# Performance work log

Measured on AMD Instinct MI355X. Metric: run time of the kernel, lower is better.

The kernel has to match this reference:

```python
import jax, jax.numpy as jnp
import numpy as np

K = 64          # number of tags, incl. BOS/EOS
V = 50000       # vocab size (excl. BOS/EOS words)
D = 128         # lexicon embedding dim
BOS_T = K - 2   # BOS tag index
EOS_T = K - 1   # EOS tag index
BATCH = 8192
L = 126         # interior words per sentence (n = L + 2 incl. BOS/EOS)
EPS = 1e-45     # smoothing added to A and B in updateAB


def setup_inputs() -> dict:
    key = jax.random.key(0)
    k1, k2, k3, k4 = jax.random.split(key, 4)
    words = jax.random.randint(k1, (BATCH, L), 0, V, dtype=jnp.int32)
    ThetaB = 0.01 * jax.random.uniform(k2, (K, D), dtype=jnp.float32)
    WA = 0.01 * jax.random.uniform(k3, (K, K), dtype=jnp.float32)
    E = jax.random.normal(k4, (V, D), dtype=jnp.float32)
    return {"words": words, "ThetaB": ThetaB, "WA": WA, "E": E}


def reference(words, ThetaB, WA, E):
    # updateAB(): A = softmax(WA) with BOS column forced to prob 0 (-inf logit)
    WAm = WA.at[:, BOS_T].set(-jnp.inf)
    A = jax.nn.softmax(WAm, axis=1) + EPS                       # [K, K]
    B = jax.nn.softmax(ThetaB @ E.T, axis=1)                    # [K, V]
    B = B.at[EOS_T, :].set(0.0).at[BOS_T, :].set(0.0) + EPS
    logA = jnp.log(A)                                           # [K, K]
    logB = jnp.log(B)                                           # [K, V]

    # Emission log-probs gathered per token: [L, B, K]
    em = jnp.swapaxes(logB.T[words], 0, 1)

    # alpha_0: one-hot (in log space) at BOS tag
    alpha0 = jnp.full((words.shape[0], K), -jnp.inf, dtype=logA.dtype)
    alpha0 = alpha0.at[:, BOS_T].set(0.0)

    def step(alpha, e):
        # alpha: [B, K] over prev tags; logsumexp over prev tag axis
        new = jax.nn.logsumexp(alpha[:, :, None] + logA[None, :, :], axis=1) + e
        return new, None

    alpha, _ = jax.lax.scan(step, alpha0, em)
    # Final transition into EOS tag (no emission): log Z per sentence, [B]
    logZ = jax.nn.logsumexp(alpha + logA[None, :, EOS_T], axis=1)
    return logZ
```

## Files before the change

kernel.cpp:

```cpp
#include <hip/hip_runtime.h>
#include <hip/hip_bf16.h>
#include <math.h>


#define KT 64
#define VV 50000
#define DD 128
#define BOS_T 62
#define EOS_T 63
#define LLEN 126
#define EPSF 1e-45f
#define SCALE_F 65536.0f
#define LOG_TOTAL_SCALE (2016.0f * 0.6931471805599453f)
#define NBLK 782
#define PBLK 784
#define TPH 21
#define NPH 6

#define BTN_OFF   0
#define A_OFF     3200000
#define SUM_OFF   3216384
#define PART_OFF  3216640

typedef short short8 __attribute__((ext_vector_type(8)));
typedef float f32x4  __attribute__((ext_vector_type(4)));
typedef float f32x2  __attribute__((ext_vector_type(2)));

union U8 { short8 v; unsigned u[4]; short s[8]; };

static __device__ inline unsigned short f2bf_u(float x) {
    __hip_bfloat16 h = __float2bfloat16(x);
    return *reinterpret_cast<unsigned short*>(&h);
}
static __device__ inline short f2bf(float x) { return (short)f2bf_u(x); }

#if __has_builtin(__builtin_amdgcn_cvt_pk_bf16_f32)
typedef __bf16 bf16x2 __attribute__((ext_vector_type(2)));
static __device__ inline unsigned pk2(float a, float b) {
    bf16x2 r = __builtin_amdgcn_cvt_pk_bf16_f32(a, b);
    return *reinterpret_cast<unsigned*>(&r);
}
#else
static __device__ inline unsigned pk2(float a, float b) {
    union { float f; unsigned u; } ua, ub;
    ua.f = a; ub.f = b;
    return ((ua.u + 0x8000u) >> 16) | ((ub.u + 0x8000u) & 0xFFFF0000u);
}
#endif
static __device__ inline float lo16(unsigned u) { union { unsigned i; float f; } c; c.i = u << 16;        return c.f; }
static __device__ inline float hi16(unsigned u) { union { unsigned i; float f; } c; c.i = u & 0xffff0000u; return c.f; }

#if __has_builtin(__builtin_amdgcn_cvt_pk_fp8_f32)
static __device__ inline unsigned pk4f8(float a, float b, float c, float d) {
    int v = __builtin_amdgcn_cvt_pk_fp8_f32(a, b, 0, false);
    v = __builtin_amdgcn_cvt_pk_fp8_f32(c, d, v, true);
    return (unsigned)v;
}
#else
static __device__ inline unsigned enc1f8(float x) {
    union { float f; unsigned u; } c; c.f = x;
    unsigned u = c.u & 0x7FFFFFFFu;
    unsigned r = u + 0x7FFFFu + ((u >> 20) & 1u);
    return ((r >> 20) - (120u << 3)) & 0x7Fu;
}
static __device__ inline unsigned pk4f8(float a, float b, float c, float d) {
    return enc1f8(a) | (enc1f8(b) << 8) | (enc1f8(c) << 16) | (enc1f8(d) << 24);
}
#endif

#if __has_builtin(__builtin_amdgcn_cvt_pk_f32_fp8)
static __device__ inline f32x2 dec2lo(unsigned w) { return __builtin_amdgcn_cvt_pk_f32_fp8((int)w, false); }
static __device__ inline f32x2 dec2hi(unsigned w) { return __builtin_amdgcn_cvt_pk_f32_fp8((int)w, true); }
#else
static __device__ inline float dec1f8(unsigned b) {
    union { unsigned u; float f; } c;
    c.u = ((b & 0x80u) << 24) | (((b & 0x7Fu) << 20) + (120u << 23));
    return c.f;
}
static __device__ inline f32x2 dec2lo(unsigned w) { f32x2 r; r.x = dec1f8(w & 0xFF); r.y = dec1f8((w >> 8) & 0xFF); return r; }
static __device__ inline f32x2 dec2hi(unsigned w) { f32x2 r; r.x = dec1f8((w >> 16) & 0xFF); r.y = dec1f8(w >> 24); return r; }
#endif

#if __has_builtin(__builtin_amdgcn_global_load_lds)
#define GLLDS(gp, lbase)                                                        \
    __builtin_amdgcn_global_load_lds(                                           \
        (__attribute__((address_space(1))) void*)const_cast<unsigned char*>(gp),\
        (__attribute__((address_space(3))) void*)(lbase), 16, 0, 0)
#else
#define GLLDS(gp, lbase)                                                        \
    do { *(uint4*)((unsigned char*)(lbase) + (threadIdx.x & 63) * 16) =         \
             *(const uint4*)(gp); } while (0)
#endif

__global__ __launch_bounds__(256) void k_emit(const float* __restrict__ ThetaB,
                                              const float* __restrict__ E,
                                              unsigned char* __restrict__ btn8,
                                              float* __restrict__ partial) {
    __shared__ float red[4][KT];
    int t    = threadIdx.x;
    int lane = t & 63;
    int w    = t >> 6;
    int n    = lane & 15;
    int q    = lane >> 4;
    int v0   = (blockIdx.x * 4 + w) * 16;

    int rowE = v0 + n;
    bool valid = rowE < VV;
    rowE = valid ? rowE : VV - 1;
    float4 ex[4][2];
#pragma unroll
    for (int kt = 0; kt < 4; ++kt) {
        const float* p = E + (size_t)rowE * DD + kt * 32 + q * 8;
        ex[kt][0] = *(const float4*)p;
        ex[kt][1] = *(const float4*)(p + 4);
    }

    short8 Th[4][4];
#pragma unroll
    for (int kt = 0; kt < 4; ++kt)
#pragma unroll
        for (int mt = 0; mt < 4; ++mt) {
            const float* p = ThetaB + (mt * 16 + n) * DD + kt * 32 + q * 8;
            float4 x = *(const float4*)p;
            float4 y = *(const float4*)(p + 4);
            U8 f;
            f.u[0] = pk2(x.x, x.y); f.u[1] = pk2(x.z, x.w);
            f.u[2] = pk2(y.x, y.y); f.u[3] = pk2(y.z, y.w);
            Th[kt][mt] = f.v;
        }

    short8 Ef[4];
#pragma unroll
    for (int kt = 0; kt < 4; ++kt) {
        U8 f;
        f.u[0] = pk2(ex[kt][0].x, ex[kt][0].y); f.u[1] = pk2(ex[kt][0].z, ex[kt][0].w);
        f.u[2] = pk2(ex[kt][1].x, ex[kt][1].y); f.u[3] = pk2(ex[kt][1].z, ex[kt][1].w);
        Ef[kt] = f.v;
    }

#pragma unroll
    for (int mt = 0; mt < 4; ++mt) {
        f32x4 C = {0.f, 0.f, 0.f, 0.f};
#pragma unroll
        for (int kt = 0; kt < 4; ++kt)
            C = __builtin_amdgcn_mfma_f32_16x16x32_bf16(Th[kt][mt], Ef[kt], C, 0, 0, 0);
        float e[4];
#pragma unroll
        for (int r = 0; r < 4; ++r) e[r] = __expf(C[r]);
        if (valid) {
            int pos = 16 * ((2 * mt + (q >> 1)) & 3) + 8 * (mt >> 1) + (q & 1) * 4;
            *(unsigned*)(btn8 + (size_t)rowE * KT + pos) = pk4f8(e[0], e[1], e[2], e[3]);
        }
#pragma unroll
        for (int r = 0; r < 4; ++r) {
            float s = valid ? e[r] : 0.0f;
            s += __shfl_xor(s, 1, 64);
            s += __shfl_xor(s, 2, 64);
            s += __shfl_xor(s, 4, 64);
            s += __shfl_xor(s, 8, 64);
            if (n == 0) red[w][mt * 16 + q * 4 + r] = s;
        }
    }
    __syncthreads();
    if (w == 0) {
        float s = red[0][lane] + red[1][lane] + red[2][lane] + red[3][lane];
        partial[lane * PBLK + blockIdx.x] = s;
    }
}

__global__ __launch_bounds__(256) void k_sumA(const float* __restrict__ partial,
                                              const float* __restrict__ WA,
                                              float* __restrict__ sumexp,
                                              float* __restrict__ A) {
    __shared__ float r[4];
    int k = blockIdx.x;
    int t = threadIdx.x;
    float s = 0.0f;
    for (int i = t; i < NBLK; i += 256) s += partial[k * PBLK + i];
#pragma unroll
    for (int off = 32; off > 0; off >>= 1) s += __shfl_xor(s, off, 64);
    if ((t & 63) == 0) r[t >> 6] = s;
    __syncthreads();
    if (t == 0) sumexp[k] = r[0] + r[1] + r[2] + r[3];
    if (t < 64) {
        float wv = WA[k * KT + t];
        float e = (t == BOS_T) ? 0.0f : __expf(wv);
        float se = e;
#pragma unroll
        for (int off = 32; off > 0; off >>= 1) se += __shfl_xor(se, off, 64);
        A[k * KT + t] = e / se + EPSF;
    }
}

__global__ __launch_bounds__(256) void k_fwd(const int* __restrict__ words,
                                             const unsigned char* __restrict__ btn8,
                                             const float* __restrict__ A,
                                             const float* __restrict__ sumexp,
                                             float* __restrict__ out) {
    __shared__ int shw[16 * LLEN];
    __shared__ __attribute__((aligned(16))) unsigned char shE[2][TPH * 1024];
    int lane = threadIdx.x & 63;
    int w    = threadIdx.x >> 6;
    int n    = lane & 15;
    int qA   = lane >> 4;
    int b0   = blockIdx.x * 16;

    {
        const uint4* src = (const uint4*)(words + (size_t)b0 * LLEN);
        uint4* dst = (uint4*)shw;
        for (int idx = threadIdx.x; idx < (16 * LLEN) / 4; idx += 256)
            dst[idx] = src[idx];
    }

    short8 Af[2][4];
    short8 B0, B1;
    if (w == 3) {
#pragma unroll
        for (int mt = 0; mt < 4; ++mt) {
            int tagn = 32 * (mt >> 1) + 8 * (n >> 2) + 4 * (mt & 1) + (n & 3);
            float s = sumexp[tagn];
            float rsn = (tagn == BOS_T || tagn == EOS_T) ? 0.0f : (SCALE_F / s);
#pragma unroll
            for (int kt = 0; kt < 2; ++kt) {
                U8 f;
#pragma unroll
                for (int j = 0; j < 8; ++j)
                    f.s[j] = f2bf(A[(kt * 32 + qA * 8 + j) * KT + tagn] * rsn);
                Af[kt][mt] = f.v;
            }
        }
        U8 z; z.u[0] = z.u[1] = z.u[2] = z.u[3] = 0;
        B0 = z.v;
        U8 o; o.u[0] = o.u[1] = o.u[2] = o.u[3] = 0;
        if (qA == 3) o.s[6] = (short)0x3F80;
        B1 = o.v;
    }
    __syncthreads();

#define PSTAGE(bb, p_)                                                        \
    do {                                                                      \
        for (int s_ = w; s_ < TPH; s_ += 3) {                                 \
            int wd_ = shw[n * LLEN + (p_) * TPH + s_];                        \
            const unsigned char* g_ = btn8 + (size_t)wd_ * KT + qA * 16;      \
            GLLDS(g_, &shE[bb][s_ * 1024]);                                   \
        }                                                                     \
        asm volatile("s_waitcnt vmcnt(0)" ::: "memory");                      \
    } while (0)

#define LDE(bb, ss) (*(const uint4*)(&shE[bb][(ss) * 1024] + lane * 16))

    if (w < 3) PSTAGE(0, 0);
    __syncthreads();

    for (int p = 0; p < NPH; ++p) {
        int b = p & 1;
        if (w < 3) {
            if (p + 1 < NPH) PSTAGE((p + 1) & 1, p + 1);
        } else {
            uint4 r0 = LDE(b, 0);
            uint4 r1 = LDE(b, 1);
#pragma unroll
            for (int s = 0; s < TPH; ++s) {
                uint4 rc = r0;
                r0 = r1;
                int s2 = (s + 2 < TPH) ? s + 2 : TPH - 1;
                r1 = LDE(b, s2);

                f32x2 d0 = dec2lo(rc.x), d1 = dec2hi(rc.x);
                f32x2 d2 = dec2lo(rc.y), d3 = dec2hi(rc.y);
                f32x2 d4 = dec2lo(rc.z), d5 = dec2hi(rc.z);
                f32x2 d6 = dec2lo(rc.w), d7 = dec2hi(rc.w);

                f32x4 C[4];
#pragma unroll
                for (int mt = 0; mt < 4; ++mt) {
                    f32x4 acc = {0.f, 0.f, 0.f, 0.f};
                    acc = __builtin_amdgcn_mfma_f32_16x16x32_bf16(Af[0][mt], B0, acc, 0, 0, 0);
                    acc = __builtin_amdgcn_mfma_f32_16x16x32_bf16(Af[1][mt], B1, acc, 0, 0, 0);
                    C[mt] = acc;
                }
                U8 f0, f1;
                f0.u[0] = pk2(C[0][0] * d0.x, C[0][1] * d0.y);
                f0.u[1] = pk2(C[0][2] * d1.x, C[0][3] * d1.y);
                f0.u[2] = pk2(C[1][0] * d2.x, C[1][1] * d2.y);
                f0.u[3] = pk2(C[1][2] * d3.x, C[1][3] * d3.y);
                f1.u[0] = pk2(C[2][0] * d4.x, C[2][1] * d4.y);
                f1.u[1] = pk2(C[2][2] * d5.x, C[2][3] * d5.y);
                f1.u[2] = pk2(C[3][0] * d6.x, C[3][1] * d6.y);
                f1.u[3] = pk2(C[3][2] * d7.x, C[3][3] * d7.y);
                B0 = f0.v; B1 = f1.v;
            }
        }
        __syncthreads();
    }

    if (w == 3) {
        short8 Afin[2];
#pragma unroll
        for (int kt = 0; kt < 2; ++kt) {
            U8 f;
#pragma unroll
            for (int j = 0; j < 8; ++j)
                f.s[j] = (n == 0) ? f2bf(A[(kt * 32 + qA * 8 + j) * KT + EOS_T]) : (short)0;
            Afin[kt] = f.v;
        }
        f32x4 Cf = {0.f, 0.f, 0.f, 0.f};
        Cf = __builtin_amdgcn_mfma_f32_16x16x32_bf16(Afin[0], B0, Cf, 0, 0, 0);
        Cf = __builtin_amdgcn_mfma_f32_16x16x32_bf16(Afin[1], B1, Cf, 0, 0, 0);
        if (qA == 0)
            out[b0 + n] = logf(Cf[0]) - LOG_TOTAL_SCALE;
    }
}

extern "C" void kernel_launch(void* const* d_in, const int* in_sizes, int n_in,
                              void* d_out, int out_size, void* d_ws, size_t ws_size,
                              hipStream_t stream) {
    const int*   words  = (const int*)d_in[0];
    const float* ThetaB = (const float*)d_in[1];
    const float* WA     = (const float*)d_in[2];
    const float* E      = (const float*)d_in[3];
    float* out = (float*)d_out;

    char* ws = (char*)d_ws;
    unsigned char* btn8 = (unsigned char*)(ws + BTN_OFF);
    float* A       = (float*)(ws + A_OFF);
    float* sumexp  = (float*)(ws + SUM_OFF);
    float* partial = (float*)(ws + PART_OFF);

    k_emit<<<NBLK, 256, 0, stream>>>(ThetaB, E, btn8, partial);
    k_sumA<<<KT, 256, 0, stream>>>(partial, WA, sumexp, A);
    k_fwd<<<8192 / 16, 256, 0, stream>>>(words, btn8, A, sumexp, out);
}
```

Before: 127.7 us.

## Fold sumexp/A reduction into emit kernel via last-block counter; split MFMA chain

Removes the separate k_sumA launch. The final block of k_emit, found with an atomic counter after a threadfence, now reduces the partial sums and builds the transition matrix A. A memset resets the counter before each launch, so the kernel launch is swapped for a memset node. Separately, the two chained MFMAs in the forward recurrence now accumulate from zero independently and are summed with a vector add, which shortens the dependent MFMA latency on the serial critical path.

```diff
diff --git a/kernel.cpp b/kernel.cpp
--- a/kernel.cpp
+++ b/kernel.cpp
@@ -21,6 +21,7 @@
 #define A_OFF     3200000
 #define SUM_OFF   3216384
 #define PART_OFF  3216640
+#define CNT_OFF   3417344
 
 typedef short short8 __attribute__((ext_vector_type(8)));
 typedef float f32x4  __attribute__((ext_vector_type(4)));
@@ -47,8 +48,6 @@
     return ((ua.u + 0x8000u) >> 16) | ((ub.u + 0x8000u) & 0xFFFF0000u);
 }
 #endif
-static __device__ inline float lo16(unsigned u) { union { unsigned i; float f; } c; c.i = u << 16;        return c.f; }
-static __device__ inline float hi16(unsigned u) { union { unsigned i; float f; } c; c.i = u & 0xffff0000u; return c.f; }
 
 #if __has_builtin(__builtin_amdgcn_cvt_pk_fp8_f32)
 static __device__ inline unsigned pk4f8(float a, float b, float c, float d) {
@@ -94,9 +93,14 @@
 
 __global__ __launch_bounds__(256) void k_emit(const float* __restrict__ ThetaB,
                                               const float* __restrict__ E,
+                                              const float* __restrict__ WA,
                                               unsigned char* __restrict__ btn8,
-                                              float* __restrict__ partial) {
+                                              float* __restrict__ partial,
+                                              float* __restrict__ sumexp,
+                                              float* __restrict__ A,
+                                              unsigned* __restrict__ counter) {
     __shared__ float red[4][KT];
+    __shared__ unsigned rank;
     int t    = threadIdx.x;
     int lane = t & 63;
     int w    = t >> 6;
@@ -166,29 +170,27 @@
         float s = red[0][lane] + red[1][lane] + red[2][lane] + red[3][lane];
         partial[lane * PBLK + blockIdx.x] = s;
     }
-}
-
-__global__ __launch_bounds__(256) void k_sumA(const float* __restrict__ partial,
-                                              const float* __restrict__ WA,
-                                              float* __restrict__ sumexp,
-                                              float* __restrict__ A) {
-    __shared__ float r[4];
-    int k = blockIdx.x;
-    int t = threadIdx.x;
-    float s = 0.0f;
-    for (int i = t; i < NBLK; i += 256) s += partial[k * PBLK + i];
-#pragma unroll
-    for (int off = 32; off > 0; off >>= 1) s += __shfl_xor(s, off, 64);
-    if ((t & 63) == 0) r[t >> 6] = s;
+
+    __threadfence();
+    if (t == 0) rank = atomicAdd(counter, 1u);
     __syncthreads();
-    if (t == 0) sumexp[k] = r[0] + r[1] + r[2] + r[3];
-    if (t < 64) {
-        float wv = WA[k * KT + t];
-        float e = (t == BOS_T) ? 0.0f : __expf(wv);
-        float se = e;
-#pragma unroll
-        for (int off = 32; off > 0; off >>= 1) se += __shfl_xor(se, off, 64);
-        A[k * KT + t] = e / se + EPSF;
+    if (rank == NBLK - 1) {
+        __threadfence();
+        int k = t & 63, part = t >> 6;
+        float s = 0.0f;
+        for (int i = part; i < NBLK; i += 4) s += partial[k * PBLK + i];
+        __syncthreads();
+        red[part][k] = s;
+        __syncthreads();
+        if (t < 64) sumexp[t] = red[0][t] + red[1][t] + red[2][t] + red[3][t];
+        for (int r = w * 16; r < w * 16 + 16; ++r) {
+            float wv = WA[r * KT + lane];
+            float e = (lane == BOS_T) ? 0.0f : __expf(wv);
+            float se = e;
+#pragma unroll
+            for (int off = 32; off > 0; off >>= 1) se += __shfl_xor(se, off, 64);
+            A[r * KT + lane] = e / se + EPSF;
+        }
     }
 }
 
@@ -274,10 +276,10 @@
                 f32x4 C[4];
 #pragma unroll
                 for (int mt = 0; mt < 4; ++mt) {
-                    f32x4 acc = {0.f, 0.f, 0.f, 0.f};
-                    acc = __builtin_amdgcn_mfma_f32_16x16x32_bf16(Af[0][mt], B0, acc, 0, 0, 0);
-                    acc = __builtin_amdgcn_mfma_f32_16x16x32_bf16(Af[1][mt], B1, acc, 0, 0, 0);
-                    C[mt] = acc;
+                    f32x4 z4 = {0.f, 0.f, 0.f, 0.f};
+                    f32x4 ca = __builtin_amdgcn_mfma_f32_16x16x32_bf16(Af[0][mt], B0, z4, 0, 0, 0);
+                    f32x4 cb = __builtin_amdgcn_mfma_f32_16x16x32_bf16(Af[1][mt], B1, z4, 0, 0, 0);
+                    C[mt] = ca + cb;
                 }
                 U8 f0, f1;
                 f0.u[0] = pk2(C[0][0] * d0.x, C[0][1] * d0.y);
@@ -323,11 +325,12 @@
 
     char* ws = (char*)d_ws;
     unsigned char* btn8 = (unsigned char*)(ws + BTN_OFF);
-    float* A       = (float*)(ws + A_OFF);
-    float* sumexp  = (float*)(ws + SUM_OFF);
-    float* partial = (float*)(ws + PART_OFF);
-
-    k_emit<<<NBLK, 256, 0, stream>>>(ThetaB, E, btn8, partial);
-    k_sumA<<<KT, 256, 0, stream>>>(partial, WA, sumexp, A);
+    float* A        = (float*)(ws + A_OFF);
+    float* sumexp   = (float*)(ws + SUM_OFF);
+    float* partial  = (float*)(ws + PART_OFF);
+    unsigned* counter = (unsigned*)(ws + CNT_OFF);
+
+    hipMemsetAsync(counter, 0, 4, stream);
+    k_emit<<<NBLK, 256, 0, stream>>>(ThetaB, E, WA, btn8, partial, sumexp, A, counter);
     k_fwd<<<8192 / 16, 256, 0, stream>>>(words, btn8, A, sumexp, out);
 }
```

After: 263.7 us. +106.5%, slower.

## Stage E tile through padded LDS and split forward-scan MFMA dependency chains

Applied to the files above, without the earlier changes.

The emission kernel now loads a 64-row block of E with coalesced float4 reads into a padded shared-memory tile, and each wave reads its rows from there. This replaces the strided per-lane global loads. Separately, in the recursion step each pair of dependent MFMAs becomes two independent MFMAs whose results are summed with vector adds, which shortens the accumulator dependency chain on the serial critical path. The cost is extra LDS use, a barrier, and extra VALU adds per step.

```diff
diff --git a/kernel.cpp b/kernel.cpp
--- a/kernel.cpp
+++ b/kernel.cpp
@@ -16,6 +16,7 @@
 #define PBLK 784
 #define TPH 21
 #define NPH 6
+#define EPITCH 132
 
 #define BTN_OFF   0
 #define A_OFF     3200000
@@ -47,8 +48,6 @@
     return ((ua.u + 0x8000u) >> 16) | ((ub.u + 0x8000u) & 0xFFFF0000u);
 }
 #endif
-static __device__ inline float lo16(unsigned u) { union { unsigned i; float f; } c; c.i = u << 16;        return c.f; }
-static __device__ inline float hi16(unsigned u) { union { unsigned i; float f; } c; c.i = u & 0xffff0000u; return c.f; }
 
 #if __has_builtin(__builtin_amdgcn_cvt_pk_fp8_f32)
 static __device__ inline unsigned pk4f8(float a, float b, float c, float d) {
@@ -96,23 +95,26 @@
                                               const float* __restrict__ E,
                                               unsigned char* __restrict__ btn8,
                                               float* __restrict__ partial) {
+    __shared__ float tile[64 * EPITCH];
     __shared__ float red[4][KT];
     int t    = threadIdx.x;
     int lane = t & 63;
     int w    = t >> 6;
     int n    = lane & 15;
     int q    = lane >> 4;
-    int v0   = (blockIdx.x * 4 + w) * 16;
-
-    int rowE = v0 + n;
-    bool valid = rowE < VV;
-    rowE = valid ? rowE : VV - 1;
-    float4 ex[4][2];
-#pragma unroll
-    for (int kt = 0; kt < 4; ++kt) {
-        const float* p = E + (size_t)rowE * DD + kt * 32 + q * 8;
-        ex[kt][0] = *(const float4*)p;
-        ex[kt][1] = *(const float4*)(p + 4);
+    int vblk = blockIdx.x * 64;
+    int v0   = vblk + w * 16;
+
+    {
+        const float4* src = (const float4*)(E + (size_t)vblk * DD);
+#pragma unroll
+        for (int i = t; i < 64 * DD / 4; i += 256) {
+            int row = i >> 5;
+            int col = i & 31;
+            float4 v = make_float4(0.f, 0.f, 0.f, 0.f);
+            if (vblk + row < VV) v = src[i];
+            *(float4*)&tile[row * EPITCH + col * 4] = v;
+        }
     }
 
     short8 Th[4][4];
@@ -128,13 +130,19 @@
             f.u[2] = pk2(y.x, y.y); f.u[3] = pk2(y.z, y.w);
             Th[kt][mt] = f.v;
         }
-
+    __syncthreads();
+
+    int rowE = v0 + n;
+    bool valid = rowE < VV;
     short8 Ef[4];
 #pragma unroll
     for (int kt = 0; kt < 4; ++kt) {
+        const float* p = &tile[(w * 16 + n) * EPITCH + kt * 32 + q * 8];
+        float4 x = *(const float4*)p;
+        float4 y = *(const float4*)(p + 4);
         U8 f;
-        f.u[0] = pk2(ex[kt][0].x, ex[kt][0].y); f.u[1] = pk2(ex[kt][0].z, ex[kt][0].w);
-        f.u[2] = pk2(ex[kt][1].x, ex[kt][1].y); f.u[3] = pk2(ex[kt][1].z, ex[kt][1].w);
+        f.u[0] = pk2(x.x, x.y); f.u[1] = pk2(x.z, x.w);
+        f.u[2] = pk2(y.x, y.y); f.u[3] = pk2(y.z, y.w);
         Ef[kt] = f.v;
     }
 
@@ -274,10 +282,10 @@
                 f32x4 C[4];
 #pragma unroll
                 for (int mt = 0; mt < 4; ++mt) {
-                    f32x4 acc = {0.f, 0.f, 0.f, 0.f};
-                    acc = __builtin_amdgcn_mfma_f32_16x16x32_bf16(Af[0][mt], B0, acc, 0, 0, 0);
-                    acc = __builtin_amdgcn_mfma_f32_16x16x32_bf16(Af[1][mt], B1, acc, 0, 0, 0);
-                    C[mt] = acc;
+                    f32x4 z4 = {0.f, 0.f, 0.f, 0.f};
+                    f32x4 ca = __builtin_amdgcn_mfma_f32_16x16x32_bf16(Af[0][mt], B0, z4, 0, 0, 0);
+                    f32x4 cb = __builtin_amdgcn_mfma_f32_16x16x32_bf16(Af[1][mt], B1, z4, 0, 0, 0);
+                    C[mt] = ca + cb;
                 }
                 U8 f0, f1;
                 f0.u[0] = pk2(C[0][0] * d0.x, C[0][1] * d0.y);
```

After: 143.2 us. +12.2%, slower.
